# Kernel tuning notes

Measured on AMD Instinct MI355X. Metric: run time of the kernel, lower is better.

The kernel has to match this reference:

```python
import jax, jax.numpy as jnp
import numpy as np

DIM = 1024
HEADS = 16
KV_HEADS = 4
HEAD_DIM = DIM // HEADS
KV_GROUPS = HEADS // KV_HEADS
SCALE = HEAD_DIM ** -0.5


def setup_inputs() -> dict:
    key = jax.random.key(0)
    ks = jax.random.split(key, 9)
    B, N = 2, 2048
    s = 0.02
    x = jax.random.normal(ks[0], (B, N, DIM), dtype=jnp.float32)
    Wq = jax.random.normal(ks[1], (DIM, HEADS * HEAD_DIM), dtype=jnp.float32) * s
    bq = jax.random.normal(ks[2], (HEADS * HEAD_DIM,), dtype=jnp.float32) * s
    Wk = jax.random.normal(ks[3], (DIM, KV_HEADS * HEAD_DIM), dtype=jnp.float32) * s
    bk = jax.random.normal(ks[4], (KV_HEADS * HEAD_DIM,), dtype=jnp.float32) * s
    Wv = jax.random.normal(ks[5], (DIM, KV_HEADS * HEAD_DIM), dtype=jnp.float32) * s
    bv = jax.random.normal(ks[6], (KV_HEADS * HEAD_DIM,), dtype=jnp.float32) * s
    Wo = jax.random.normal(ks[7], (HEADS * HEAD_DIM, DIM), dtype=jnp.float32) * s
    bo = jax.random.normal(ks[8], (DIM,), dtype=jnp.float32) * s
    return {"x": x, "Wq": Wq, "bq": bq, "Wk": Wk, "bk": bk,
            "Wv": Wv, "bv": bv, "Wo": Wo, "bo": bo}


def reference(x, Wq, bq, Wk, bk, Wv, bv, Wo, bo):
    B, N, _ = x.shape
    # projections -> [B, H, N, D]
    q = (x @ Wq + bq).reshape(B, N, HEADS, HEAD_DIM).transpose(0, 2, 1, 3)
    k = (x @ Wk + bk).reshape(B, N, KV_HEADS, HEAD_DIM).transpose(0, 2, 1, 3)
    v = (x @ Wv + bv).reshape(B, N, KV_HEADS, HEAD_DIM).transpose(0, 2, 1, 3)
    # repeat_kv: [B, KV, N, D] -> [B, KV*G, N, D]
    k = jnp.repeat(k, KV_GROUPS, axis=1)
    v = jnp.repeat(v, KV_GROUPS, axis=1)
    attn = jnp.einsum('bhqd,bhkd->bhqk', q, k) * SCALE
    attn = jax.nn.softmax(attn, axis=-1)
    out = jnp.einsum('bhqk,bhkd->bhqd', attn, v)
    out = out.transpose(0, 2, 1, 3).reshape(B, N, HEADS * HEAD_DIM)
    return out @ Wo + bo
```

## Files before the change

### kernel.cpp

```cpp
#include <hip/hip_runtime.h>
#include <hip/hip_bf16.h>
#include <stdint.h>

#define DIM   1024
#define HEADS 16
#define KVH   4
#define HD    64
#define SEQ   2048
#define BATCH 2
#define MTOT  (BATCH*SEQ)
#define NT    (SEQ/32)

#define QSCALE 0.18033688011112042f

typedef __attribute__((ext_vector_type(8)))  short v8s;
typedef __attribute__((ext_vector_type(4)))  float v4f;
typedef __attribute__((ext_vector_type(16))) float f32x16;

static __device__ __forceinline__ short f2bf(float v) {
    __hip_bfloat16 h = __float2bfloat16(v);
    return *reinterpret_cast<short*>(&h);
}

static __device__ __forceinline__ void gload_lds16(const void* g, void* l) {
    __builtin_amdgcn_global_load_lds(
        (const __attribute__((address_space(1))) unsigned int*)g,
        (__attribute__((address_space(3))) unsigned int*)l, 16, 0, 0);
}

__global__ __launch_bounds__(256) void k_cvt(const float* __restrict__ in,
                                             short* __restrict__ out, int n4) {
    int i = blockIdx.x * 256 + threadIdx.x;
    if (i >= n4) return;
    float4 v = reinterpret_cast<const float4*>(in)[i];
    short4 o;
    o.x = f2bf(v.x); o.y = f2bf(v.y); o.z = f2bf(v.z); o.w = f2bf(v.w);
    reinterpret_cast<short4*>(out)[i] = o;
}

__global__ __launch_bounds__(256) void k_transpose_w(const float* __restrict__ W,
                                                     short* __restrict__ Wt,
                                                     int rows, int cols) {
    __shared__ float tile[32][33];
    int c0 = blockIdx.x * 32, r0 = blockIdx.y * 32;
    int tx = threadIdx.x & 31;
    int ty = threadIdx.x >> 5;
#pragma unroll
    for (int i = 0; i < 4; ++i)
        tile[ty + i*8][tx] = W[(size_t)(r0 + ty + i*8) * cols + c0 + tx];
    __syncthreads();
#pragma unroll
    for (int i = 0; i < 4; ++i)
        Wt[(size_t)(c0 + ty + i*8) * rows + r0 + tx] = f2bf(tile[tx][ty + i*8]);
}

template<int MODE>
__global__ __launch_bounds__(256)
void k_gemm(const short* __restrict__ A, const short* __restrict__ Bt,
            const float* __restrict__ bias1, const float* __restrict__ bias2,
            void* __restrict__ Cout, int K, int Nout) {
    __shared__ short As[128 * 64];
    __shared__ short Bs[128 * 64];
    const int tid  = threadIdx.x;
    const int lane = tid & 63;
    const int wave = tid >> 6;
    const int bm = blockIdx.x * 128;
    const int bn = blockIdx.y * 128;
    const int wm = (wave >> 1) * 64;
    const int wn = (wave & 1) * 64;
    const int lo = lane & 15, hi = lane >> 4;
    v4f acc[4][4] = {};
    const int nkt = K >> 6;
    for (int kt = 0; kt < nkt; ++kt) {
        __syncthreads();
#pragma unroll
        for (int i = 0; i < 4; ++i) {
            int c = i * 256 + tid;
            int row = c >> 3, col = c & 7;
            int4 va = *reinterpret_cast<const int4*>(A  + (size_t)(bm + row) * K + kt*64 + col*8);
            *reinterpret_cast<int4*>(reinterpret_cast<char*>(As) + row*128 + ((col*16) ^ ((row & 7) << 4))) = va;
            int4 vb = *reinterpret_cast<const int4*>(Bt + (size_t)(bn + row) * K + kt*64 + col*8);
            *reinterpret_cast<int4*>(reinterpret_cast<char*>(Bs) + row*128 + ((col*16) ^ ((row & 7) << 4))) = vb;
        }
        __syncthreads();
#pragma unroll
        for (int ks = 0; ks < 2; ++ks) {
            v8s af[4], bfr[4];
#pragma unroll
            for (int mf = 0; mf < 4; ++mf) {
                int row = wm + mf*16 + lo;
                af[mf] = *reinterpret_cast<const v8s*>(reinterpret_cast<const char*>(As)
                           + row*128 + ((ks*64 + hi*16) ^ ((row & 7) << 4)));
            }
#pragma unroll
            for (int nf = 0; nf < 4; ++nf) {
                int row = wn + nf*16 + lo;
                bfr[nf] = *reinterpret_cast<const v8s*>(reinterpret_cast<const char*>(Bs)
                           + row*128 + ((ks*64 + hi*16) ^ ((row & 7) << 4)));
            }
#pragma unroll
            for (int mf = 0; mf < 4; ++mf)
#pragma unroll
                for (int nf = 0; nf < 4; ++nf)
                    acc[mf][nf] = __builtin_amdgcn_mfma_f32_16x16x32_bf16(af[mf], bfr[nf], acc[mf][nf], 0, 0, 0);
        }
    }
#pragma unroll
    for (int nf = 0; nf < 4; ++nf) {
        int col = bn + wn + nf*16 + lo;
#pragma unroll
        for (int mf = 0; mf < 4; ++mf) {
#pragma unroll
            for (int j = 0; j < 4; ++j) {
                int grow = bm + wm + mf*16 + hi*4 + j;
                float acv = acc[mf][nf][j];
                if (MODE == 1) {
                    reinterpret_cast<float*>(Cout)[(size_t)grow * Nout + col] = acv + bias1[col];
                } else if (MODE == 2) {
                    float val = acv + bias1[grow];
                    reinterpret_cast<short*>(Cout)[((size_t)(col >> 11) * 256 + grow) * 2048 + (col & 2047)] = f2bf(val);
                } else {
                    int b = grow >> 11, n = grow & 2047;
                    if (col < 1024) {
                        int hh = col >> 6, d = col & 63;
                        float val = (acv + bias1[col]) * QSCALE;
                        reinterpret_cast<short*>(Cout)[((size_t)(b * HEADS + hh) * SEQ + n) * HD + d] = f2bf(val);
                    } else {
                        int cc = col - 1024;
                        int kvh = cc >> 6, d = cc & 63;
                        float val = acv + bias2[cc];
                        reinterpret_cast<short*>(Cout)[4194304 + ((size_t)(b * KVH + kvh) * SEQ + n) * HD + d] = f2bf(val);
                    }
                }
            }
        }
    }
}

__global__ __launch_bounds__(256, 2)
void k_attn(const short* __restrict__ Q, const short* __restrict__ K,
            const short* __restrict__ Vt, short* __restrict__ AO) {
    __shared__ int4 KbL[2][256];
    __shared__ int4 VbL[2][256];
    const int tid  = threadIdx.x;
    const int lane = tid & 63;
    const int w    = tid >> 6;
    const int l31 = lane & 31, hi2 = (lane >> 5) & 1;
    const int id  = blockIdx.x;
    const int g   = id & 7;
    const int b   = g >> 2, kvh = g & 3;
    const int qt  = id >> 3;
    const int h   = kvh * 4 + w;
    const int q0  = qt * 32;

    const char* Kg = (const char*)(K  + (size_t)(b * KVH + kvh) * SEQ * HD);
    const char* Vg = (const char*)(Vt + (size_t)(b * KVH + kvh) * HD * SEQ);
    const short* Qb = Q + ((size_t)(b * HEADS + h) * SEQ + q0) * HD;

    const int krow  = w * 8 + (lane >> 3);
    const int ksrc  = krow * 128 + (((lane & 7) ^ (krow & 7)) << 4);
    const int vd    = w * 16 + (lane >> 2);
    const int vchk  = (lane & 3) ^ ((vd >> 1) & 3);
    const size_t vsrc = (size_t)vd * (SEQ * 2) + (size_t)vchk * 16;

    v8s qf[4];
#pragma unroll
    for (int c = 0; c < 4; ++c)
        qf[c] = *reinterpret_cast<const v8s*>(Qb + (size_t)l31 * HD + c * 16 + hi2 * 8);

    f32x16 acc0 = {}, acc1 = {};
    float mrun = -1e30f, lsum = 0.f;

    gload_lds16(Kg + ksrc,              (char*)KbL[0] + w * 1024);
    gload_lds16(Vg + vsrc,              (char*)VbL[0] + w * 1024);
    __syncthreads();

    int cur = 0;
    for (int kt = 0; kt < NT; ++kt) {
        if (kt + 1 < NT) {
            gload_lds16(Kg + (size_t)(kt + 1) * 4096 + ksrc, (char*)KbL[cur ^ 1] + w * 1024);
            gload_lds16(Vg + vsrc + (size_t)(kt + 1) * 64,   (char*)VbL[cur ^ 1] + w * 1024);
        }
        const char* Kl = (const char*)KbL[cur];
        const char* Vl = (const char*)VbL[cur];

        f32x16 s = {};
#pragma unroll
        for (int c = 0; c < 4; ++c) {
            v8s kf = *reinterpret_cast<const v8s*>(Kl + l31 * 128 + (((2*c + hi2) ^ (l31 & 7)) << 4));
            s = __builtin_amdgcn_mfma_f32_32x32x16_bf16(kf, qf[c], s, 0, 0, 0);
        }
        float m0 = fmaxf(fmaxf(s[0],  s[1]),  fmaxf(s[2],  s[3]));
        float m1 = fmaxf(fmaxf(s[4],  s[5]),  fmaxf(s[6],  s[7]));
        float m2 = fmaxf(fmaxf(s[8],  s[9]),  fmaxf(s[10], s[11]));
        float m3 = fmaxf(fmaxf(s[12], s[13]), fmaxf(s[14], s[15]));
        float pmax = fmaxf(fmaxf(m0, m1), fmaxf(m2, m3));
        pmax = fmaxf(pmax, __shfl_xor(pmax, 32));
        if (!__all(pmax <= mrun + 8.f)) {
            float mnew = fmaxf(mrun, pmax);
            float sc = exp2f(mrun - mnew);
#pragma unroll
            for (int r = 0; r < 16; ++r) { acc0[r] *= sc; acc1[r] *= sc; }
            lsum *= sc;
            mrun = mnew;
        }
#pragma unroll
        for (int r = 0; r < 16; ++r) s[r] = exp2f(s[r] - mrun);
        float a0 = (s[0] + s[1]) + (s[2]  + s[3]);
        float a1 = (s[4] + s[5]) + (s[6]  + s[7]);
        float a2 = (s[8] + s[9]) + (s[10] + s[11]);
        float a3 = (s[12]+ s[13])+ (s[14] + s[15]);
        float ls = (a0 + a1) + (a2 + a3);
        lsum += ls + __shfl_xor(ls, 32);

        int pk[8];
#pragma unroll
        for (int i = 0; i < 8; ++i) {
            int r;
            asm("v_cvt_pk_bf16_f32 %0, %1, %2" : "=v"(r) : "v"(s[2*i]), "v"(s[2*i+1]));
            pk[i] = r;
        }
        int u[8];
#pragma unroll
        for (int i = 0; i < 2; ++i) {
            int p0 = pk[4*i+0], p1 = pk[4*i+1], p2 = pk[4*i+2], p3 = pk[4*i+3];
            int o0 = __shfl_xor(p0, 32), o1 = __shfl_xor(p1, 32);
            int o2 = __shfl_xor(p2, 32), o3 = __shfl_xor(p3, 32);
            u[4*i+0] = hi2 ? o2 : p0;
            u[4*i+1] = hi2 ? o3 : p1;
            u[4*i+2] = hi2 ? p2 : o0;
            u[4*i+3] = hi2 ? p3 : o1;
        }
        union { int i4[4]; v8s v; } pb0, pb1;
        pb0.i4[0] = u[0]; pb0.i4[1] = u[1]; pb0.i4[2] = u[2]; pb0.i4[3] = u[3];
        pb1.i4[0] = u[4]; pb1.i4[1] = u[5]; pb1.i4[2] = u[6]; pb1.i4[3] = u[7];

        const int vx = (l31 >> 1) & 3;
        {
            v8s vf0 = *reinterpret_cast<const v8s*>(Vl + l31 * 64        + ((hi2       ^ vx) << 4));
            acc0 = __builtin_amdgcn_mfma_f32_32x32x16_bf16(vf0, pb0.v, acc0, 0, 0, 0);
            v8s vf1 = *reinterpret_cast<const v8s*>(Vl + (32 + l31) * 64 + ((hi2       ^ vx) << 4));
            acc1 = __builtin_amdgcn_mfma_f32_32x32x16_bf16(vf1, pb0.v, acc1, 0, 0, 0);
            v8s vf2 = *reinterpret_cast<const v8s*>(Vl + l31 * 64        + (((2 + hi2) ^ vx) << 4));
            acc0 = __builtin_amdgcn_mfma_f32_32x32x16_bf16(vf2, pb1.v, acc0, 0, 0, 0);
            v8s vf3 = *reinterpret_cast<const v8s*>(Vl + (32 + l31) * 64 + (((2 + hi2) ^ vx) << 4));
            acc1 = __builtin_amdgcn_mfma_f32_32x32x16_bf16(vf3, pb1.v, acc1, 0, 0, 0);
        }
        __syncthreads();
        cur ^= 1;
    }

    float rinv = 1.f / lsum;
    short* Ao = AO + ((size_t)(b * SEQ + q0 + l31)) * DIM + h * HD;
#pragma unroll
    for (int rg = 0; rg < 4; ++rg) {
        short4 st0, st1;
        st0.x = f2bf(acc0[rg*4+0] * rinv); st0.y = f2bf(acc0[rg*4+1] * rinv);
        st0.z = f2bf(acc0[rg*4+2] * rinv); st0.w = f2bf(acc0[rg*4+3] * rinv);
        *reinterpret_cast<short4*>(Ao + rg*8 + hi2*4) = st0;
        st1.x = f2bf(acc1[rg*4+0] * rinv); st1.y = f2bf(acc1[rg*4+1] * rinv);
        st1.z = f2bf(acc1[rg*4+2] * rinv); st1.w = f2bf(acc1[rg*4+3] * rinv);
        *reinterpret_cast<short4*>(Ao + 32 + rg*8 + hi2*4) = st1;
    }
}

extern "C" void kernel_launch(void* const* d_in, const int* in_sizes, int n_in,
                              void* d_out, int out_size, void* d_ws, size_t ws_size,
                              hipStream_t stream) {
    const float* x  = (const float*)d_in[0];
    const float* Wq = (const float*)d_in[1];
    const float* bq = (const float*)d_in[2];
    const float* Wk = (const float*)d_in[3];
    const float* bk = (const float*)d_in[4];
    const float* Wv = (const float*)d_in[5];
    const float* bv = (const float*)d_in[6];
    const float* Wo = (const float*)d_in[7];
    const float* bo = (const float*)d_in[8];
    float* out = (float*)d_out;

    char* w = (char*)d_ws;
    size_t off = 0;
    auto alloc = [&](size_t bytes) { void* p = w + off; off += (bytes + 255) & ~(size_t)255; return p; };
    short* xb   = (short*)alloc((size_t)MTOT * DIM * 2);
    short* WqkT = (short*)alloc((size_t)(DIM + KVH*HD) * DIM * 2);
    short* WvT  = (short*)alloc((size_t)(KVH*HD) * DIM * 2);
    short* WoT  = (short*)alloc((size_t)DIM * DIM * 2);
    short* QK   = (short*)alloc((size_t)(BATCH*HEADS*SEQ*HD + BATCH*KVH*SEQ*HD) * 2);
    short* VtG  = (short*)alloc((size_t)BATCH * KVH * HD * SEQ * 2);
    short* AO   = (short*)alloc((size_t)MTOT * DIM * 2);

    short* Qh = QK;
    short* Kh = QK + (size_t)BATCH * HEADS * SEQ * HD;

    k_cvt<<<dim3((MTOT * DIM / 4 + 255) / 256), dim3(256), 0, stream>>>(x, xb, MTOT * DIM / 4);
    k_transpose_w<<<dim3(DIM/32,      DIM/32), dim3(256), 0, stream>>>(Wq, WqkT,             DIM, DIM);
    k_transpose_w<<<dim3((KVH*HD)/32, DIM/32), dim3(256), 0, stream>>>(Wk, WqkT + DIM*DIM,   DIM, KVH*HD);
    k_transpose_w<<<dim3((KVH*HD)/32, DIM/32), dim3(256), 0, stream>>>(Wv, WvT,              DIM, KVH*HD);
    k_transpose_w<<<dim3(DIM/32,      DIM/32), dim3(256), 0, stream>>>(Wo, WoT,              DIM, DIM);

    k_gemm<3><<<dim3(MTOT/128, (DIM + KVH*HD)/128), dim3(256), 0, stream>>>(
        xb, WqkT, bq, bk, (void*)QK, DIM, DIM + KVH*HD);
    k_gemm<2><<<dim3((KVH*HD)/128, MTOT/128), dim3(256), 0, stream>>>(
        WvT, xb, bv, nullptr, (void*)VtG, DIM, MTOT);

    k_attn<<<dim3(BATCH * KVH * (SEQ/32)), dim3(256), 0, stream>>>(Qh, Kh, VtG, AO);

    k_gemm<1><<<dim3(MTOT/128, DIM/128), dim3(256), 0, stream>>>(
        AO, WoT, bo, nullptr, (void*)out, DIM, DIM);
}
```

Before: 242.4 us.

## Merge weight transposes, use direct-to-LDS loads in GEMM, enlarge attention KV tiles

The four weight-transpose launches become a single launch whose z index selects the matrix, cutting launch overhead. The GEMM tile loads now use global_load_lds in place of register round-trips, with an XOR swizzle applied on the global side. The attention kernel stages 128-key K/V tiles per double-buffer step instead of 32, giving fewer barriers per tile, and raises the occupancy hint to 4 blocks per SM. Larger LDS buffers (64KB per block) may not actually allow 4 blocks per CU, and the new swizzle patterns have to match the reads exactly.

```diff
diff --git a/kernel.cpp b/kernel.cpp
--- a/kernel.cpp
+++ b/kernel.cpp
@@ -9,7 +9,6 @@
 #define SEQ   2048
 #define BATCH 2
 #define MTOT  (BATCH*SEQ)
-#define NT    (SEQ/32)
 
 #define QSCALE 0.18033688011112042f
 
@@ -38,11 +37,19 @@
     reinterpret_cast<short4*>(out)[i] = o;
 }
 
-__global__ __launch_bounds__(256) void k_transpose_w(const float* __restrict__ W,
-                                                     short* __restrict__ Wt,
-                                                     int rows, int cols) {
+__global__ __launch_bounds__(256) void k_transpose_all(
+        const float* __restrict__ Wq, const float* __restrict__ Wk,
+        const float* __restrict__ Wv, const float* __restrict__ Wo,
+        short* __restrict__ WqkT, short* __restrict__ WvT, short* __restrict__ WoT) {
+    const int z = blockIdx.z;
+    const float* W; short* Wt; int rows, cols;
+    if      (z == 0) { W = Wq; Wt = WqkT;            rows = DIM; cols = DIM;    }
+    else if (z == 1) { W = Wk; Wt = WqkT + DIM*DIM;  rows = DIM; cols = KVH*HD; }
+    else if (z == 2) { W = Wv; Wt = WvT;             rows = DIM; cols = KVH*HD; }
+    else             { W = Wo; Wt = WoT;             rows = DIM; cols = DIM;    }
+    int c0 = blockIdx.x * 32, r0 = blockIdx.y * 32;
+    if (c0 >= cols || r0 >= rows) return;
     __shared__ float tile[32][33];
-    int c0 = blockIdx.x * 32, r0 = blockIdx.y * 32;
     int tx = threadIdx.x & 31;
     int ty = threadIdx.x >> 5;
 #pragma unroll
@@ -69,18 +76,19 @@
     const int wm = (wave >> 1) * 64;
     const int wn = (wave & 1) * 64;
     const int lo = lane & 15, hi = lane >> 4;
+    const int l8 = lane & 7, lr = lane >> 3;
+    const int sslot = (l8 ^ lr) << 4;
     v4f acc[4][4] = {};
     const int nkt = K >> 6;
     for (int kt = 0; kt < nkt; ++kt) {
         __syncthreads();
 #pragma unroll
         for (int i = 0; i < 4; ++i) {
-            int c = i * 256 + tid;
-            int row = c >> 3, col = c & 7;
-            int4 va = *reinterpret_cast<const int4*>(A  + (size_t)(bm + row) * K + kt*64 + col*8);
-            *reinterpret_cast<int4*>(reinterpret_cast<char*>(As) + row*128 + ((col*16) ^ ((row & 7) << 4))) = va;
-            int4 vb = *reinterpret_cast<const int4*>(Bt + (size_t)(bn + row) * K + kt*64 + col*8);
-            *reinterpret_cast<int4*>(reinterpret_cast<char*>(Bs) + row*128 + ((col*16) ^ ((row & 7) << 4))) = vb;
+            int row = i * 32 + wave * 8 + lr;
+            gload_lds16((const char*)(A  + (size_t)(bm + row) * K + kt*64) + sslot,
+                        (char*)As + i*4096 + wave*1024);
+            gload_lds16((const char*)(Bt + (size_t)(bn + row) * K + kt*64) + sslot,
+                        (char*)Bs + i*4096 + wave*1024);
         }
         __syncthreads();
 #pragma unroll
@@ -137,11 +145,11 @@
     }
 }
 
-__global__ __launch_bounds__(256, 2)
+__global__ __launch_bounds__(256, 4)
 void k_attn(const short* __restrict__ Q, const short* __restrict__ K,
             const short* __restrict__ Vt, short* __restrict__ AO) {
-    __shared__ int4 KbL[2][256];
-    __shared__ int4 VbL[2][256];
+    __shared__ int4 KbL[2][1024];
+    __shared__ int4 VbL[2][1024];
     const int tid  = threadIdx.x;
     const int lane = tid & 63;
     const int w    = tid >> 6;
@@ -157,12 +165,6 @@
     const char* Vg = (const char*)(Vt + (size_t)(b * KVH + kvh) * HD * SEQ);
     const short* Qb = Q + ((size_t)(b * HEADS + h) * SEQ + q0) * HD;
 
-    const int krow  = w * 8 + (lane >> 3);
-    const int ksrc  = krow * 128 + (((lane & 7) ^ (krow & 7)) << 4);
-    const int vd    = w * 16 + (lane >> 2);
-    const int vchk  = (lane & 3) ^ ((vd >> 1) & 3);
-    const size_t vsrc = (size_t)vd * (SEQ * 2) + (size_t)vchk * 16;
-
     v8s qf[4];
 #pragma unroll
     for (int c = 0; c < 4; ++c)
@@ -170,81 +172,93 @@
 
     f32x16 acc0 = {}, acc1 = {};
     float mrun = -1e30f, lsum = 0.f;
-
-    gload_lds16(Kg + ksrc,              (char*)KbL[0] + w * 1024);
-    gload_lds16(Vg + vsrc,              (char*)VbL[0] + w * 1024);
+    const int sr = (l31 & 7) ^ ((l31 & 8) >> 1);
+
+    auto stage = [&](int bi, int T) {
+#pragma unroll
+        for (int i = 0; i < 4; ++i) {
+            int r  = w * 32 + i * 8 + (lane >> 3);
+            int ks = ((lane & 7) ^ (r & 7) ^ ((r & 8) >> 1)) << 4;
+            gload_lds16(Kg + (size_t)T * 16384 + (size_t)r * 128 + ks,
+                        (char*)KbL[bi] + w * 4096 + i * 1024);
+            int d  = w * 16 + i * 4 + (lane >> 4);
+            int cs = (((lane & 15) ^ (d & 7) ^ ((d & 8) >> 1))) << 4;
+            gload_lds16(Vg + (size_t)d * 4096 + (size_t)T * 256 + cs,
+                        (char*)VbL[bi] + w * 4096 + i * 1024);
+        }
+    };
+
+    stage(0, 0);
     __syncthreads();
-
     int cur = 0;
-    for (int kt = 0; kt < NT; ++kt) {
-        if (kt + 1 < NT) {
-            gload_lds16(Kg + (size_t)(kt + 1) * 4096 + ksrc, (char*)KbL[cur ^ 1] + w * 1024);
-            gload_lds16(Vg + vsrc + (size_t)(kt + 1) * 64,   (char*)VbL[cur ^ 1] + w * 1024);
-        }
+    for (int T = 0; T < SEQ / 128; ++T) {
+        if (T + 1 < SEQ / 128) stage(cur ^ 1, T + 1);
         const char* Kl = (const char*)KbL[cur];
         const char* Vl = (const char*)VbL[cur];
-
-        f32x16 s = {};
-#pragma unroll
-        for (int c = 0; c < 4; ++c) {
-            v8s kf = *reinterpret_cast<const v8s*>(Kl + l31 * 128 + (((2*c + hi2) ^ (l31 & 7)) << 4));
-            s = __builtin_amdgcn_mfma_f32_32x32x16_bf16(kf, qf[c], s, 0, 0, 0);
-        }
-        float m0 = fmaxf(fmaxf(s[0],  s[1]),  fmaxf(s[2],  s[3]));
-        float m1 = fmaxf(fmaxf(s[4],  s[5]),  fmaxf(s[6],  s[7]));
-        float m2 = fmaxf(fmaxf(s[8],  s[9]),  fmaxf(s[10], s[11]));
-        float m3 = fmaxf(fmaxf(s[12], s[13]), fmaxf(s[14], s[15]));
-        float pmax = fmaxf(fmaxf(m0, m1), fmaxf(m2, m3));
-        pmax = fmaxf(pmax, __shfl_xor(pmax, 32));
-        if (!__all(pmax <= mrun + 8.f)) {
-            float mnew = fmaxf(mrun, pmax);
-            float sc = exp2f(mrun - mnew);
-#pragma unroll
-            for (int r = 0; r < 16; ++r) { acc0[r] *= sc; acc1[r] *= sc; }
-            lsum *= sc;
-            mrun = mnew;
-        }
-#pragma unroll
-        for (int r = 0; r < 16; ++r) s[r] = exp2f(s[r] - mrun);
-        float a0 = (s[0] + s[1]) + (s[2]  + s[3]);
-        float a1 = (s[4] + s[5]) + (s[6]  + s[7]);
-        float a2 = (s[8] + s[9]) + (s[10] + s[11]);
-        float a3 = (s[12]+ s[13])+ (s[14] + s[15]);
-        float ls = (a0 + a1) + (a2 + a3);
-        lsum += ls + __shfl_xor(ls, 32);
-
-        int pk[8];
-#pragma unroll
-        for (int i = 0; i < 8; ++i) {
-            int r;
-            asm("v_cvt_pk_bf16_f32 %0, %1, %2" : "=v"(r) : "v"(s[2*i]), "v"(s[2*i+1]));
-            pk[i] = r;
-        }
-        int u[8];
-#pragma unroll
-        for (int i = 0; i < 2; ++i) {
-            int p0 = pk[4*i+0], p1 = pk[4*i+1], p2 = pk[4*i+2], p3 = pk[4*i+3];
-            int o0 = __shfl_xor(p0, 32), o1 = __shfl_xor(p1, 32);
-            int o2 = __shfl_xor(p2, 32), o3 = __shfl_xor(p3, 32);
-            u[4*i+0] = hi2 ? o2 : p0;
-            u[4*i+1] = hi2 ? o3 : p1;
-            u[4*i+2] = hi2 ? p2 : o0;
-            u[4*i+3] = hi2 ? p3 : o1;
-        }
-        union { int i4[4]; v8s v; } pb0, pb1;
-        pb0.i4[0] = u[0]; pb0.i4[1] = u[1]; pb0.i4[2] = u[2]; pb0.i4[3] = u[3];
-        pb1.i4[0] = u[4]; pb1.i4[1] = u[5]; pb1.i4[2] = u[6]; pb1.i4[3] = u[7];
-
-        const int vx = (l31 >> 1) & 3;
-        {
-            v8s vf0 = *reinterpret_cast<const v8s*>(Vl + l31 * 64        + ((hi2       ^ vx) << 4));
-            acc0 = __builtin_amdgcn_mfma_f32_32x32x16_bf16(vf0, pb0.v, acc0, 0, 0, 0);
-            v8s vf1 = *reinterpret_cast<const v8s*>(Vl + (32 + l31) * 64 + ((hi2       ^ vx) << 4));
-            acc1 = __builtin_amdgcn_mfma_f32_32x32x16_bf16(vf1, pb0.v, acc1, 0, 0, 0);
-            v8s vf2 = *reinterpret_cast<const v8s*>(Vl + l31 * 64        + (((2 + hi2) ^ vx) << 4));
-            acc0 = __builtin_amdgcn_mfma_f32_32x32x16_bf16(vf2, pb1.v, acc0, 0, 0, 0);
-            v8s vf3 = *reinterpret_cast<const v8s*>(Vl + (32 + l31) * 64 + (((2 + hi2) ^ vx) << 4));
-            acc1 = __builtin_amdgcn_mfma_f32_32x32x16_bf16(vf3, pb1.v, acc1, 0, 0, 0);
+#pragma unroll
+        for (int st = 0; st < 4; ++st) {
+            f32x16 s = {};
+#pragma unroll
+            for (int c = 0; c < 4; ++c) {
+                v8s kf = *reinterpret_cast<const v8s*>(
+                    Kl + (st*32 + l31) * 128 + (((2*c + hi2) ^ sr) << 4));
+                s = __builtin_amdgcn_mfma_f32_32x32x16_bf16(kf, qf[c], s, 0, 0, 0);
+            }
+            float m0 = fmaxf(fmaxf(s[0],  s[1]),  fmaxf(s[2],  s[3]));
+            float m1 = fmaxf(fmaxf(s[4],  s[5]),  fmaxf(s[6],  s[7]));
+            float m2 = fmaxf(fmaxf(s[8],  s[9]),  fmaxf(s[10], s[11]));
+            float m3 = fmaxf(fmaxf(s[12], s[13]), fmaxf(s[14], s[15]));
+            float pmax = fmaxf(fmaxf(m0, m1), fmaxf(m2, m3));
+            pmax = fmaxf(pmax, __shfl_xor(pmax, 32));
+            if (!__all(pmax <= mrun + 8.f)) {
+                float mnew = fmaxf(mrun, pmax);
+                float sc = exp2f(mrun - mnew);
+#pragma unroll
+                for (int r = 0; r < 16; ++r) { acc0[r] *= sc; acc1[r] *= sc; }
+                lsum *= sc;
+                mrun = mnew;
+            }
+#pragma unroll
+            for (int r = 0; r < 16; ++r) s[r] = exp2f(s[r] - mrun);
+            float a0 = (s[0] + s[1]) + (s[2]  + s[3]);
+            float a1 = (s[4] + s[5]) + (s[6]  + s[7]);
+            float a2 = (s[8] + s[9]) + (s[10] + s[11]);
+            float a3 = (s[12]+ s[13])+ (s[14] + s[15]);
+            float ls = (a0 + a1) + (a2 + a3);
+            lsum += ls + __shfl_xor(ls, 32);
+
+            int pk[8];
+#pragma unroll
+            for (int i = 0; i < 8; ++i) {
+                int r;
+                asm("v_cvt_pk_bf16_f32 %0, %1, %2" : "=v"(r) : "v"(s[2*i]), "v"(s[2*i+1]));
+                pk[i] = r;
+            }
+            int u[8];
+#pragma unroll
+            for (int i = 0; i < 2; ++i) {
+                int p0 = pk[4*i+0], p1 = pk[4*i+1], p2 = pk[4*i+2], p3 = pk[4*i+3];
+                int o0 = __shfl_xor(p0, 32), o1 = __shfl_xor(p1, 32);
+                int o2 = __shfl_xor(p2, 32), o3 = __shfl_xor(p3, 32);
+                u[4*i+0] = hi2 ? o2 : p0;
+                u[4*i+1] = hi2 ? o3 : p1;
+                u[4*i+2] = hi2 ? p2 : o0;
+                u[4*i+3] = hi2 ? p3 : o1;
+            }
+            union { int i4[4]; v8s v; } pb0, pb1;
+            pb0.i4[0] = u[0]; pb0.i4[1] = u[1]; pb0.i4[2] = u[2]; pb0.i4[3] = u[3];
+            pb1.i4[0] = u[4]; pb1.i4[1] = u[5]; pb1.i4[2] = u[6]; pb1.i4[3] = u[7];
+
+            {
+                v8s vf0 = *reinterpret_cast<const v8s*>(Vl + l31 * 256        + (((st*4     + hi2) ^ sr) << 4));
+                acc0 = __builtin_amdgcn_mfma_f32_32x32x16_bf16(vf0, pb0.v, acc0, 0, 0, 0);
+                v8s vf1 = *reinterpret_cast<const v8s*>(Vl + (32 + l31) * 256 + (((st*4     + hi2) ^ sr) << 4));
+                acc1 = __builtin_amdgcn_mfma_f32_32x32x16_bf16(vf1, pb0.v, acc1, 0, 0, 0);
+                v8s vf2 = *reinterpret_cast<const v8s*>(Vl + l31 * 256        + (((st*4 + 2 + hi2) ^ sr) << 4));
+                acc0 = __builtin_amdgcn_mfma_f32_32x32x16_bf16(vf2, pb1.v, acc0, 0, 0, 0);
+                v8s vf3 = *reinterpret_cast<const v8s*>(Vl + (32 + l31) * 256 + (((st*4 + 2 + hi2) ^ sr) << 4));
+                acc1 = __builtin_amdgcn_mfma_f32_32x32x16_bf16(vf3, pb1.v, acc1, 0, 0, 0);
+            }
         }
         __syncthreads();
         cur ^= 1;
@@ -293,10 +307,7 @@
     short* Kh = QK + (size_t)BATCH * HEADS * SEQ * HD;
 
     k_cvt<<<dim3((MTOT * DIM / 4 + 255) / 256), dim3(256), 0, stream>>>(x, xb, MTOT * DIM / 4);
-    k_transpose_w<<<dim3(DIM/32,      DIM/32), dim3(256), 0, stream>>>(Wq, WqkT,             DIM, DIM);
-    k_transpose_w<<<dim3((KVH*HD)/32, DIM/32), dim3(256), 0, stream>>>(Wk, WqkT + DIM*DIM,   DIM, KVH*HD);
-    k_transpose_w<<<dim3((KVH*HD)/32, DIM/32), dim3(256), 0, stream>>>(Wv, WvT,              DIM, KVH*HD);
-    k_transpose_w<<<dim3(DIM/32,      DIM/32), dim3(256), 0, stream>>>(Wo, WoT,              DIM, DIM);
+    k_transpose_all<<<dim3(32, 32, 4), dim3(256), 0, stream>>>(Wq, Wk, Wv, Wo, WqkT, WvT, WoT);
 
     k_gemm<3><<<dim3(MTOT/128, (DIM + KVH*HD)/128), dim3(256), 0, stream>>>(
         xb, WqkT, bq, bk, (void*)QK, DIM, DIM + KVH*HD);
```

After: 235.4 us. 2.9% less time.
